# Kernel tuning notes

Hardware: AMD Instinct MI355X
Metric: run time of the kernel (lower is better)

Reference implementation:

```python
import jax, jax.numpy as jnp
import numpy as np

B, S, D = 1, 2048, 4096
N_Q, N_KV, HD = 32, 8, 128
N_REP = N_Q // N_KV
WINDOW = 1024
NEG = -1e9


def setup_inputs() -> dict:
    key = jax.random.key(0)
    ks = jax.random.split(key, 6)
    x = jax.random.normal(ks[0], (B, S, D), dtype=jnp.float32)
    # RoPE frequencies (Llama-style): theta = 10000^{-2i/HD}
    inv_freq = 1.0 / (10000.0 ** (np.arange(0, HD, 2, dtype=np.float32) / HD))
    t = np.arange(S, dtype=np.float32)
    ang = np.outer(t, inv_freq)  # [S, HD//2]
    freqs_cos = jnp.asarray(np.cos(ang), dtype=jnp.float32)
    freqs_sin = jnp.asarray(np.sin(ang), dtype=jnp.float32)
    # additive causal mask [S, S]: 0 on/below diag, -1e9 above
    mask = jnp.where(jnp.tril(jnp.ones((S, S), dtype=bool)), 0.0, NEG).astype(jnp.float32)
    scale = 0.02
    w_q = jax.random.normal(ks[1], (D, N_Q * HD), dtype=jnp.float32) * scale
    w_k = jax.random.normal(ks[2], (D, N_KV * HD), dtype=jnp.float32) * scale
    w_v = jax.random.normal(ks[3], (D, N_KV * HD), dtype=jnp.float32) * scale
    w_o = jax.random.normal(ks[4], (N_Q * HD, D), dtype=jnp.float32) * scale
    return {"x": x, "freqs_cos": freqs_cos, "freqs_sin": freqs_sin, "mask": mask,
            "w_q": w_q, "w_k": w_k, "w_v": w_v, "w_o": w_o}


def _rope(t, cos, sin):
    # t: [B, S, H, HD]; cos/sin: [S, HD//2] -> complex multiply on pairs
    tp = t.reshape(*t.shape[:-1], HD // 2, 2)
    e, o = tp[..., 0], tp[..., 1]
    c = cos[None, :, None, :]
    s = sin[None, :, None, :]
    re = e * c - o * s
    ro = e * s + o * c
    return jnp.stack([re, ro], axis=-1).reshape(t.shape)


def reference(x, freqs_cos, freqs_sin, mask, w_q, w_k, w_v, w_o):
    b, s, _ = x.shape
    xq = (x @ w_q).reshape(b, s, N_Q, HD)
    xk = (x @ w_k).reshape(b, s, N_KV, HD)
    xv = (x @ w_v).reshape(b, s, N_KV, HD)
    xq = _rope(xq, freqs_cos, freqs_sin)
    xk = _rope(xk, freqs_cos, freqs_sin)
    # GQA head repeat
    keys = jnp.repeat(xk, N_REP, axis=2)    # [b, s, N_Q, HD]
    values = jnp.repeat(xv, N_REP, axis=2)
    q = xq.transpose(0, 2, 1, 3)            # [b, h, s, hd]
    k = keys.transpose(0, 2, 1, 3)
    v = values.transpose(0, 2, 1, 3)
    scores = jnp.einsum('bhqd,bhkd->bhqk', q, k) / jnp.sqrt(jnp.float32(HD))
    scores = scores + mask[None, None, :, :]
    # sliding-window band: attend only to keys within WINDOW positions back
    idx = jnp.arange(s)
    diff = idx[:, None] - idx[None, :]
    sliding = (diff >= 0) & (diff < WINDOW)
    scores = jnp.where(sliding[None, None, :, :], scores, NEG)
    probs = jax.nn.softmax(scores, axis=-1).astype(q.dtype)
    out = jnp.einsum('bhqk,bhkd->bhqd', probs, v)
    out = out.transpose(0, 2, 1, 3).reshape(b, s, N_Q * HD)
    return out @ w_o
```

## Files before the change

### kernel.cpp

```cpp
#include <hip/hip_runtime.h>

typedef unsigned short u16;
typedef unsigned int u32;
typedef __bf16 bf16x8 __attribute__((ext_vector_type(8)));
typedef __bf16 bf16x4 __attribute__((ext_vector_type(4)));
typedef float f32x4 __attribute__((ext_vector_type(4)));

#define MFMA16(a, b, c) __builtin_amdgcn_mfma_f32_16x16x32_bf16(a, b, c, 0, 0, 0)

__device__ __forceinline__ u16 f2bf(float f) {
  u32 u = __float_as_uint(f);
  u += 0x7FFFu + ((u >> 16) & 1u);
  return (u16)(u >> 16);
}
__device__ __forceinline__ float bf2f(u16 h) {
  return __uint_as_float(((u32)h) << 16);
}

__device__ __forceinline__ void gload_lds16(const u16* g, u16* l) {
  __builtin_amdgcn_global_load_lds((__attribute__((address_space(1))) void*)g,
                                   (__attribute__((address_space(3))) void*)l,
                                   16, 0, 0);
}

__global__ __launch_bounds__(256) void cvt_x(const float* __restrict__ in,
                                             u16* __restrict__ out) {
  int i = (blockIdx.x * 256 + threadIdx.x) * 4;
  float4 v = *(const float4*)&in[i];
  ushort4 o;
  o.x = f2bf(v.x);
  o.y = f2bf(v.y);
  o.z = f2bf(v.z);
  o.w = f2bf(v.w);
  *(ushort4*)&out[i] = o;
}

__global__ __launch_bounds__(256) void tbf_f2b(const float* __restrict__ in,
                                               u16* __restrict__ out,
                                               int ldin, int ldout) {
  __shared__ float tile[64][65];
  const int t = threadIdx.x;
  const int c4 = t & 15;
  const int rb = t >> 4;
  const int r0 = blockIdx.y * 64;
  const int c0 = blockIdx.x * 64;
#pragma unroll
  for (int p = 0; p < 4; p++) {
    int r = p * 16 + rb;
    float4 v = *(const float4*)&in[(size_t)(r0 + r) * ldin + c0 + c4 * 4];
    tile[r][c4 * 4 + 0] = v.x;
    tile[r][c4 * 4 + 1] = v.y;
    tile[r][c4 * 4 + 2] = v.z;
    tile[r][c4 * 4 + 3] = v.w;
  }
  __syncthreads();
#pragma unroll
  for (int p = 0; p < 4; p++) {
    int oc = p * 16 + rb;
    ushort4 v;
    v.x = f2bf(tile[c4 * 4 + 0][oc]);
    v.y = f2bf(tile[c4 * 4 + 1][oc]);
    v.z = f2bf(tile[c4 * 4 + 2][oc]);
    v.w = f2bf(tile[c4 * 4 + 3][oc]);
    *(ushort4*)&out[(size_t)(c0 + oc) * ldout + r0 + c4 * 4] = v;
  }
}

__global__ __launch_bounds__(256) void tbf_b(const u16* __restrict__ in,
                                             u16* __restrict__ out,
                                             int ldin, int ldout) {
  __shared__ u16 tile[64][68];
  const int t = threadIdx.x;
  const int c4 = t & 15;
  const int rb = t >> 4;
  const int r0 = blockIdx.y * 64;
  const int c0 = blockIdx.x * 64;
#pragma unroll
  for (int p = 0; p < 4; p++) {
    int r = p * 16 + rb;
    ushort4 v = *(const ushort4*)&in[(size_t)(r0 + r) * ldin + c0 + c4 * 4];
    *(ushort4*)&tile[r][c4 * 4] = v;
  }
  __syncthreads();
#pragma unroll
  for (int p = 0; p < 4; p++) {
    int oc = p * 16 + rb;
    ushort4 v;
    v.x = tile[c4 * 4 + 0][oc];
    v.y = tile[c4 * 4 + 1][oc];
    v.z = tile[c4 * 4 + 2][oc];
    v.w = tile[c4 * 4 + 3][oc];
    *(ushort4*)&out[(size_t)(c0 + oc) * ldout + r0 + c4 * 4] = v;
  }
}

template <int BN, int F32OUT>
__global__ __launch_bounds__(512, 2) void gemmp(const u16* __restrict__ A,
                                                const u16* __restrict__ B,
                                                void* __restrict__ Cv,
                                                int K, int ldc) {
  constexpr int BM = 256;
  constexpr int R = 4;
  constexpr int C = BN / 32;
  constexpr int CH = C / 2;
  constexpr int LA = BM / 64;
  constexpr int LB = BN / 64;
  __shared__ __attribute__((aligned(16))) u16 As[2][BM * 64];
  __shared__ __attribute__((aligned(16))) u16 Bs[2][BN * 64];
  const int tid = threadIdx.x;
  const int wave = tid >> 6;
  const int lane = tid & 63;
  const int l16 = lane & 15;
  const int quad = lane >> 4;
  const int wm = wave >> 1;
  const int wn = wave & 1;
  const int id = blockIdx.x;
  const int bm = (id & 7) * BM;
  const int bn0 = (id >> 3) * BN;

  const u16* srcA[LA];
#pragma unroll
  for (int m = 0; m < LA; m++) {
    int c = m * 512 + tid;
    int r = c >> 3;
    int hl = (c & 7) ^ (r & 7);
    srcA[m] = A + (size_t)(bm + r) * K + hl * 8;
  }
  const u16* srcB[LB];
#pragma unroll
  for (int m = 0; m < LB; m++) {
    int c = m * 512 + tid;
    int r = c >> 3;
    int hl = (c & 7) ^ (r & 7);
    srcB[m] = B + (size_t)(bn0 + r) * K + hl * 8;
  }

  f32x4 acc[R][C];
#pragma unroll
  for (int i = 0; i < R; i++)
#pragma unroll
    for (int j = 0; j < C; j++) acc[i][j] = (f32x4){0.f, 0.f, 0.f, 0.f};

  auto stage = [&](int ko, int buf) {
#pragma unroll
    for (int m = 0; m < LA; m++)
      gload_lds16(srcA[m] + ko, &As[buf][(m * 512 + tid) * 8]);
#pragma unroll
    for (int m = 0; m < LB; m++)
      gload_lds16(srcB[m] + ko, &Bs[buf][(m * 512 + tid) * 8]);
  };

  const int NT = K >> 6;
  stage(0, 0);
  for (int t = 0; t < NT; ++t) {
    if (t + 1 < NT) {
      stage((t + 1) << 6, (t + 1) & 1);
      if constexpr (LA + LB == 7)
        asm volatile("s_waitcnt vmcnt(7)" ::: "memory");
      else
        asm volatile("s_waitcnt vmcnt(6)" ::: "memory");
    } else {
      asm volatile("s_waitcnt vmcnt(0)" ::: "memory");
    }
    __builtin_amdgcn_sched_barrier(0);
    __builtin_amdgcn_s_barrier();
    __builtin_amdgcn_sched_barrier(0);

    const u16* as = &As[t & 1][0];
    const u16* bs = &Bs[t & 1][0];
    bf16x8 afr[R];
#pragma unroll
    for (int ks = 0; ks < 2; ks++) {
#pragma unroll
      for (int ph = 0; ph < 2; ph++) {
        if (ph == 0) {
#pragma unroll
          for (int i = 0; i < R; i++) {
            int row = wm * 64 + i * 16 + l16;
            afr[i] = *(const bf16x8*)
                &as[row * 64 + (((ks * 4 + quad) ^ (row & 7)) << 3)];
          }
        }
        bf16x8 bfr[CH];
#pragma unroll
        for (int j = 0; j < CH; j++) {
          int row = wn * (C * 16) + (ph * CH + j) * 16 + l16;
          bfr[j] = *(const bf16x8*)
              &bs[row * 64 + (((ks * 4 + quad) ^ (row & 7)) << 3)];
        }
        __builtin_amdgcn_s_setprio(1);
#pragma unroll
        for (int i = 0; i < R; i++)
#pragma unroll
          for (int j = 0; j < CH; j++)
            acc[i][ph * CH + j] = MFMA16(afr[i], bfr[j], acc[i][ph * CH + j]);
        __builtin_amdgcn_s_setprio(0);
        __builtin_amdgcn_sched_barrier(0);
        __builtin_amdgcn_s_barrier();
        __builtin_amdgcn_sched_barrier(0);
      }
    }
  }

  const int crow0 = bm + wm * 64;
  const int ccol0 = bn0 + wn * (C * 16);
  if constexpr (F32OUT) {
    float* Cp = (float*)Cv;
#pragma unroll
    for (int i = 0; i < R; i++)
#pragma unroll
      for (int j = 0; j < C; j++)
#pragma unroll
        for (int rr = 0; rr < 4; rr++) {
          int row = crow0 + i * 16 + quad * 4 + rr;
          int col = ccol0 + j * 16 + l16;
          Cp[(size_t)row * ldc + col] = acc[i][j][rr];
        }
  } else {
    u16* Cp = (u16*)Cv;
#pragma unroll
    for (int i = 0; i < R; i++)
#pragma unroll
      for (int j = 0; j < C; j++)
#pragma unroll
        for (int rr = 0; rr < 4; rr++) {
          int row = crow0 + i * 16 + quad * 4 + rr;
          int col = ccol0 + j * 16 + l16;
          Cp[(size_t)row * ldc + col] = f2bf(acc[i][j][rr]);
        }
  }
}

__global__ __launch_bounds__(256) void rope_k(u16* __restrict__ qkv,
                                              const float* __restrict__ fc,
                                              const float* __restrict__ fs) {
  int idx = blockIdx.x * 256 + threadIdx.x;
  int j = idx & 63;
  int rem = idx >> 6;
  int head = rem % 40;
  int s = rem / 40;
  float c = fc[s * 64 + j];
  float sn = fs[s * 64 + j];
  int col = (head < 32) ? (head * 128 + 2 * j) : (4096 + (head - 32) * 128 + 2 * j);
  u32* p = (u32*)&qkv[(size_t)s * 6144 + col];
  u32 v = *p;
  float e = bf2f((u16)(v & 0xFFFFu));
  float o = bf2f((u16)(v >> 16));
  float re = e * c - o * sn;
  float ro = e * sn + o * c;
  *p = (u32)f2bf(re) | ((u32)f2bf(ro) << 16);
}

__global__ __launch_bounds__(256) void attn_k(const u16* __restrict__ qkv,
                                              const u16* __restrict__ vt,
                                              u16* __restrict__ outb) {
  __shared__ __attribute__((aligned(16))) u16 Kb[2][32 * 128];
  __shared__ __attribute__((aligned(16))) u16 Vb[2][128 * 32];
  __shared__ __attribute__((aligned(16))) u16 plds[4][32 * 36];
  const int h = blockIdx.x;
  const int q0 = blockIdx.y * 128;
  const int t = threadIdx.x;
  const int wave = t >> 6;
  const int lane = t & 63;
  const int l16 = lane & 15;
  const int quad = lane >> 4;
  const int hkv = h >> 2;
  const int qw = q0 + wave * 32;
  u16* myp = &plds[wave][0];

  bf16x8 qa[2][4];
#pragma unroll
  for (int i = 0; i < 2; i++)
#pragma unroll
    for (int kc = 0; kc < 4; kc++)
      qa[i][kc] = *(const bf16x8*)&qkv[(size_t)(qw + i * 16 + l16) * 6144 +
                                       h * 128 + kc * 32 + quad * 8];

  f32x4 o[2][8];
#pragma unroll
  for (int i = 0; i < 2; i++)
#pragma unroll
    for (int d = 0; d < 8; d++) o[i][d] = (f32x4){0.f, 0.f, 0.f, 0.f};
  float lloc[2][4] = {{0.f, 0.f, 0.f, 0.f}, {0.f, 0.f, 0.f, 0.f}};

  const int kb_start = (q0 - 1023 > 0 ? q0 - 1023 : 0) & ~31;
  const int kb_last = q0 + 96;
  const float sc = 0.08838834764831845f;

  const int kr0 = t >> 4, kc0s = t & 15;
  const int kr1 = (256 + t) >> 4, kc1s = t & 15;
  const int vr0 = t >> 2, vc0s = t & 3;
  const int vr1 = (256 + t) >> 2, vc1s = t & 3;
  const u16* kg = qkv + 4096 + hkv * 128;
  const u16* vg = vt + (size_t)hkv * 128 * 2048;

#define STAGE(kb_, nb_)                                                        \
  do {                                                                         \
    int kb__ = (kb_);                                                          \
    gload_lds16(&kg[(size_t)(kb__ + kr0) * 6144 + (kc0s ^ (kr0 & 15)) * 8],    \
                &Kb[nb_][t * 8]);                                              \
    gload_lds16(&kg[(size_t)(kb__ + kr1) * 6144 + (kc1s ^ (kr1 & 15)) * 8],    \
                &Kb[nb_][2048 + t * 8]);                                       \
    gload_lds16(&vg[(size_t)vr0 * 2048 + kb__ + (vc0s ^ (vr0 & 3)) * 8],       \
                &Vb[nb_][t * 8]);                                              \
    gload_lds16(&vg[(size_t)vr1 * 2048 + kb__ + (vc1s ^ (vr1 & 3)) * 8],       \
                &Vb[nb_][2048 + t * 8]);                                       \
  } while (0)

  STAGE(kb_start, 0);
  int cur = 0;

  for (int kb = kb_start; kb <= kb_last; kb += 32) {
    __syncthreads();
    if (kb + 32 <= kb_last) STAGE(kb + 32, cur ^ 1);
    const u16* kcur = &Kb[cur][0];
    const u16* vcur = &Vb[cur][0];

    f32x4 s0[2] = {(f32x4){0.f, 0.f, 0.f, 0.f}, (f32x4){0.f, 0.f, 0.f, 0.f}};
    f32x4 s1[2] = {(f32x4){0.f, 0.f, 0.f, 0.f}, (f32x4){0.f, 0.f, 0.f, 0.f}};
#pragma unroll
    for (int kc = 0; kc < 4; kc++) {
      int ch = ((kc * 4 + quad) ^ l16) * 8;
      bf16x8 b0 = *(const bf16x8*)&kcur[l16 * 128 + ch];
      bf16x8 b1 = *(const bf16x8*)&kcur[(l16 + 16) * 128 + ch];
      s0[0] = MFMA16(qa[0][kc], b0, s0[0]);
      s1[0] = MFMA16(qa[0][kc], b1, s1[0]);
      s0[1] = MFMA16(qa[1][kc], b0, s0[1]);
      s1[1] = MFMA16(qa[1][kc], b1, s1[1]);
    }

    float p0[2][4], p1[2][4];
    bool fast = (kb + 31 <= qw) && (qw + 31 - kb <= 1023);
    if (fast) {
#pragma unroll
      for (int i = 0; i < 2; i++)
#pragma unroll
        for (int r = 0; r < 4; r++) {
          p0[i][r] = __expf(s0[i][r] * sc);
          p1[i][r] = __expf(s1[i][r] * sc);
        }
    } else {
#pragma unroll
      for (int i = 0; i < 2; i++)
#pragma unroll
        for (int r = 0; r < 4; r++) {
          int row = qw + i * 16 + quad * 4 + r;
          int col0 = kb + l16;
          int col1 = col0 + 16;
          bool v0 = (col0 <= row) && (row - col0 < 1024);
          bool v1 = (col1 <= row) && (row - col1 < 1024);
          p0[i][r] = v0 ? __expf(s0[i][r] * sc) : 0.f;
          p1[i][r] = v1 ? __expf(s1[i][r] * sc) : 0.f;
        }
    }
#pragma unroll
    for (int i = 0; i < 2; i++)
#pragma unroll
      for (int r = 0; r < 4; r++) {
        lloc[i][r] += p0[i][r] + p1[i][r];
        myp[(i * 16 + quad * 4 + r) * 36 + l16] = f2bf(p0[i][r]);
        myp[(i * 16 + quad * 4 + r) * 36 + l16 + 16] = f2bf(p1[i][r]);
      }
    asm volatile("s_waitcnt lgkmcnt(0)" ::: "memory");
    bf16x8 pa[2];
#pragma unroll
    for (int i = 0; i < 2; i++) {
      bf16x4 lo = *(const bf16x4*)&myp[(i * 16 + l16) * 36 + quad * 8];
      bf16x4 hi = *(const bf16x4*)&myp[(i * 16 + l16) * 36 + quad * 8 + 4];
#pragma unroll
      for (int j = 0; j < 4; j++) {
        pa[i][j] = lo[j];
        pa[i][j + 4] = hi[j];
      }
    }
#pragma unroll
    for (int d = 0; d < 8; d++) {
      int rv = l16 + 16 * d;
      bf16x8 vb = *(const bf16x8*)&vcur[rv * 32 + ((quad ^ (l16 & 3)) * 8)];
      o[0][d] = MFMA16(pa[0], vb, o[0][d]);
      o[1][d] = MFMA16(pa[1], vb, o[1][d]);
    }
    cur ^= 1;
  }

#pragma unroll
  for (int i = 0; i < 2; i++) {
    float inv[4];
#pragma unroll
    for (int r = 0; r < 4; r++) {
      float l = lloc[i][r];
#pragma unroll
      for (int m = 8; m >= 1; m >>= 1) l += __shfl_xor(l, m, 64);
      inv[r] = 1.0f / l;
    }
#pragma unroll
    for (int d = 0; d < 8; d++)
#pragma unroll
      for (int r = 0; r < 4; r++) {
        int row = qw + i * 16 + quad * 4 + r;
        outb[(size_t)row * 4096 + h * 128 + d * 16 + l16] =
            f2bf(o[i][d][r] * inv[r]);
      }
  }
#undef STAGE
}

extern "C" void kernel_launch(void* const* d_in, const int* in_sizes, int n_in,
                              void* d_out, int out_size, void* d_ws, size_t ws_size,
                              hipStream_t stream) {
  const float* x = (const float*)d_in[0];
  const float* fc = (const float*)d_in[1];
  const float* fs = (const float*)d_in[2];
  const float* wq = (const float*)d_in[4];
  const float* wk = (const float*)d_in[5];
  const float* wv = (const float*)d_in[6];
  const float* wo = (const float*)d_in[7];
  float* outp = (float*)d_out;
  char* ws = (char*)d_ws;
  u16* xb = (u16*)(ws);
  u16* wqkvT = (u16*)(ws + 16777216);
  u16* qkvb = (u16*)(ws + 67108864);
  u16* vtb = (u16*)(ws + 92274688);
  u16* aout = (u16*)(ws + 96468992);

  cvt_x<<<8192, 256, 0, stream>>>(x, xb);
  tbf_f2b<<<dim3(64, 64), 256, 0, stream>>>(wq, wqkvT, 4096, 4096);
  tbf_f2b<<<dim3(16, 64), 256, 0, stream>>>(wk, wqkvT + (size_t)4096 * 4096,
                                            1024, 4096);
  tbf_f2b<<<dim3(16, 64), 256, 0, stream>>>(wv, wqkvT + (size_t)5120 * 4096,
                                            1024, 4096);
  gemmp<192, 0><<<256, 512, 0, stream>>>(xb, wqkvT, qkvb, 4096, 6144);
  rope_k<<<20480, 256, 0, stream>>>(qkvb, fc, fs);
  tbf_b<<<dim3(16, 32), 256, 0, stream>>>(qkvb + 5120, vtb, 6144, 2048);
  tbf_f2b<<<dim3(64, 64), 256, 0, stream>>>(wo, wqkvT, 4096, 4096);
  attn_k<<<dim3(32, 16), 256, 0, stream>>>(qkvb, vtb, aout);
  gemmp<128, 1><<<256, 512, 0, stream>>>(aout, wqkvT, outp, 4096, 4096);
}
```

Measured before the change: 526.7 us.

## Restructure GEMM into 8-phase interleaved load/MFMA schedule with 2x4 wave layout

Replaces the double-buffered GEMM main loop with a hand-scheduled eight-phase ping-pong. Each phase issues a fraction of the next tile's global-to-LDS loads between register fragment reads and an MFMA cluster, with explicit barriers and vmcnt waits. Waves are regrouped as 2x4, so each wave computes 128 rows by NC*16 columns, which changes fragment reuse. The aim is to hide global load latency and LDS reads behind MFMA work. In exchange, the per-wave accumulator count grows and the wait counts are fragile and must match the issued loads exactly.

New measurement: 481.0 us. 1.1x faster.

```diff
diff --git a/kernel.cpp b/kernel.cpp
--- a/kernel.cpp
+++ b/kernel.cpp
@@ -95,140 +95,229 @@
 }
 
 template <int BN, int F32OUT>
-__global__ __launch_bounds__(512, 2) void gemmp(const u16* __restrict__ A,
+__global__ __launch_bounds__(512, 2) void gemm8(const u16* __restrict__ A,
                                                 const u16* __restrict__ B,
                                                 void* __restrict__ Cv,
                                                 int K, int ldc) {
-  constexpr int BM = 256;
-  constexpr int R = 4;
-  constexpr int C = BN / 32;
-  constexpr int CH = C / 2;
-  constexpr int LA = BM / 64;
-  constexpr int LB = BN / 64;
-  __shared__ __attribute__((aligned(16))) u16 As[2][BM * 64];
+  constexpr int NC = BN / 64;
+  __shared__ __attribute__((aligned(16))) u16 As[2][256 * 64];
   __shared__ __attribute__((aligned(16))) u16 Bs[2][BN * 64];
   const int tid = threadIdx.x;
   const int wave = tid >> 6;
   const int lane = tid & 63;
   const int l16 = lane & 15;
   const int quad = lane >> 4;
-  const int wm = wave >> 1;
-  const int wn = wave & 1;
+  const int wm = wave >> 2;
+  const int wc = wave & 3;
   const int id = blockIdx.x;
-  const int bm = (id & 7) * BM;
+  const int bm = (id & 7) * 256;
   const int bn0 = (id >> 3) * BN;
 
-  const u16* srcA[LA];
-#pragma unroll
-  for (int m = 0; m < LA; m++) {
+  const u16* srcA[4];
+#pragma unroll
+  for (int m = 0; m < 4; m++) {
     int c = m * 512 + tid;
     int r = c >> 3;
     int hl = (c & 7) ^ (r & 7);
     srcA[m] = A + (size_t)(bm + r) * K + hl * 8;
   }
-  const u16* srcB[LB];
-#pragma unroll
-  for (int m = 0; m < LB; m++) {
+  const u16* srcB[NC];
+#pragma unroll
+  for (int m = 0; m < NC; m++) {
     int c = m * 512 + tid;
     int r = c >> 3;
     int hl = (c & 7) ^ (r & 7);
     srcB[m] = B + (size_t)(bn0 + r) * K + hl * 8;
   }
 
-  f32x4 acc[R][C];
-#pragma unroll
-  for (int i = 0; i < R; i++)
-#pragma unroll
-    for (int j = 0; j < C; j++) acc[i][j] = (f32x4){0.f, 0.f, 0.f, 0.f};
-
-  auto stage = [&](int ko, int buf) {
-#pragma unroll
-    for (int m = 0; m < LA; m++)
-      gload_lds16(srcA[m] + ko, &As[buf][(m * 512 + tid) * 8]);
-#pragma unroll
-    for (int m = 0; m < LB; m++)
-      gload_lds16(srcB[m] + ko, &Bs[buf][(m * 512 + tid) * 8]);
+  f32x4 acc[8][NC];
+#pragma unroll
+  for (int i = 0; i < 8; i++)
+#pragma unroll
+    for (int j = 0; j < NC; j++) acc[i][j] = (f32x4){0.f, 0.f, 0.f, 0.f};
+
+#define STA(u, koff, buf) \
+  gload_lds16(srcA[u] + (koff), &As[buf][((u) * 512 + tid) * 8])
+#define STB(u, koff, buf) \
+  gload_lds16(srcB[u] + (koff), &Bs[buf][((u) * 512 + tid) * 8])
+#define SB __builtin_amdgcn_sched_barrier(0)
+#define MID                                          \
+  SB;                                                \
+  __builtin_amdgcn_s_barrier();                      \
+  asm volatile("s_waitcnt lgkmcnt(0)" ::: "memory"); \
+  SB
+#define END                     \
+  SB;                           \
+  __builtin_amdgcn_s_barrier(); \
+  SB
+
+  bf16x8 aR[2][4], bR0[NC], bR1[NC];
+  auto rdA = [&](const u16* s, int mh) {
+#pragma unroll
+    for (int ks = 0; ks < 2; ks++)
+#pragma unroll
+      for (int ii = 0; ii < 4; ii++) {
+        int row = wm * 128 + mh * 64 + ii * 16 + l16;
+        aR[ks][ii] = *(const bf16x8*)
+            &s[row * 64 + (((ks * 4 + quad) ^ (row & 7)) << 3)];
+      }
   };
-
-  const int NT = K >> 6;
-  stage(0, 0);
-  for (int t = 0; t < NT; ++t) {
-    if (t + 1 < NT) {
-      stage((t + 1) << 6, (t + 1) & 1);
-      if constexpr (LA + LB == 7)
-        asm volatile("s_waitcnt vmcnt(7)" ::: "memory");
+  auto rdB = [&](const u16* s, int ks, bf16x8(&bR)[NC]) {
+#pragma unroll
+    for (int j = 0; j < NC; j++) {
+      int row = wc * (NC * 16) + j * 16 + l16;
+      bR[j] = *(const bf16x8*)
+          &s[row * 64 + (((ks * 4 + quad) ^ (row & 7)) << 3)];
+    }
+  };
+  auto cl = [&](bf16x8(&a4)[4], bf16x8(&bR)[NC], int mh) {
+    __builtin_amdgcn_s_setprio(1);
+#pragma unroll
+    for (int ii = 0; ii < 4; ii++)
+#pragma unroll
+      for (int j = 0; j < NC; j++)
+        acc[mh * 4 + ii][j] = MFMA16(a4[ii], bR[j], acc[mh * 4 + ii][j]);
+    __builtin_amdgcn_s_setprio(0);
+  };
+
+#pragma unroll
+  for (int u = 0; u < 4; u++) STA(u, 0, 0);
+#pragma unroll
+  for (int u = 0; u < NC; u++) STB(u, 0, 0);
+#pragma unroll
+  for (int u = 0; u < NC; u++) STB(u, 64, 1);
+  if constexpr (NC == 3)
+    asm volatile("s_waitcnt vmcnt(3)" ::: "memory");
+  else
+    asm volatile("s_waitcnt vmcnt(2)" ::: "memory");
+  END;
+
+  const int NP = K >> 7;
+  for (int p = 0; p < NP; ++p) {
+    const int kT1 = p * 128 + 64;
+    const int kT2 = p * 128 + 128;
+    const int kT3 = p * 128 + 192;
+    const bool more = (p + 1 < NP);
+    const u16* as0 = &As[0][0];
+    const u16* bs0 = &Bs[0][0];
+    const u16* as1 = &As[1][0];
+    const u16* bs1 = &Bs[1][0];
+
+    rdA(as0, 0);
+    rdB(bs0, 0, bR0);
+    STA(0, kT1, 1);
+    STA(1, kT1, 1);
+    MID;
+    cl(aR[0], bR0, 0);
+    END;
+    rdB(bs0, 1, bR1);
+    STA(2, kT1, 1);
+    STA(3, kT1, 1);
+    MID;
+    cl(aR[1], bR1, 0);
+    END;
+    rdA(as0, 1);
+    if (more) {
+      STB(0, kT2, 0);
+      STB(1, kT2, 0);
+    }
+    MID;
+    cl(aR[1], bR1, 1);
+    END;
+    if (more) {
+      if constexpr (NC == 3) {
+        STB(2, kT2, 0);
+        STA(0, kT2, 0);
+      } else {
+        STA(0, kT2, 0);
+        STA(1, kT2, 0);
+      }
+    }
+    MID;
+    cl(aR[0], bR0, 1);
+    SB;
+    if (more)
+      asm volatile("s_waitcnt vmcnt(4)" ::: "memory");
+    else
+      asm volatile("s_waitcnt vmcnt(0)" ::: "memory");
+    END;
+
+    rdA(as1, 0);
+    rdB(bs1, 0, bR0);
+    if (more) {
+      if constexpr (NC == 3) {
+        STA(1, kT2, 0);
+        STA(2, kT2, 0);
+      } else {
+        STA(2, kT2, 0);
+        STA(3, kT2, 0);
+      }
+    }
+    MID;
+    cl(aR[0], bR0, 0);
+    END;
+    rdB(bs1, 1, bR1);
+    if (more) {
+      if constexpr (NC == 3) STA(3, kT2, 0);
+    }
+    MID;
+    cl(aR[1], bR1, 0);
+    END;
+    rdA(as1, 1);
+    if (more) {
+      STB(0, kT3, 1);
+      STB(1, kT3, 1);
+    }
+    MID;
+    cl(aR[1], bR1, 1);
+    END;
+    if (more) {
+      if constexpr (NC == 3) STB(2, kT3, 1);
+    }
+    MID;
+    cl(aR[0], bR0, 1);
+    SB;
+    if (more) {
+      if constexpr (NC == 3)
+        asm volatile("s_waitcnt vmcnt(3)" ::: "memory");
       else
-        asm volatile("s_waitcnt vmcnt(6)" ::: "memory");
-    } else {
-      asm volatile("s_waitcnt vmcnt(0)" ::: "memory");
-    }
-    __builtin_amdgcn_sched_barrier(0);
-    __builtin_amdgcn_s_barrier();
-    __builtin_amdgcn_sched_barrier(0);
-
-    const u16* as = &As[t & 1][0];
-    const u16* bs = &Bs[t & 1][0];
-    bf16x8 afr[R];
-#pragma unroll
-    for (int ks = 0; ks < 2; ks++) {
-#pragma unroll
-      for (int ph = 0; ph < 2; ph++) {
-        if (ph == 0) {
-#pragma unroll
-          for (int i = 0; i < R; i++) {
-            int row = wm * 64 + i * 16 + l16;
-            afr[i] = *(const bf16x8*)
-                &as[row * 64 + (((ks * 4 + quad) ^ (row & 7)) << 3)];
-          }
-        }
-        bf16x8 bfr[CH];
-#pragma unroll
-        for (int j = 0; j < CH; j++) {
-          int row = wn * (C * 16) + (ph * CH + j) * 16 + l16;
-          bfr[j] = *(const bf16x8*)
-              &bs[row * 64 + (((ks * 4 + quad) ^ (row & 7)) << 3)];
-        }
-        __builtin_amdgcn_s_setprio(1);
-#pragma unroll
-        for (int i = 0; i < R; i++)
-#pragma unroll
-          for (int j = 0; j < CH; j++)
-            acc[i][ph * CH + j] = MFMA16(afr[i], bfr[j], acc[i][ph * CH + j]);
-        __builtin_amdgcn_s_setprio(0);
-        __builtin_amdgcn_sched_barrier(0);
-        __builtin_amdgcn_s_barrier();
-        __builtin_amdgcn_sched_barrier(0);
-      }
-    }
-  }
-
-  const int crow0 = bm + wm * 64;
-  const int ccol0 = bn0 + wn * (C * 16);
+        asm volatile("s_waitcnt vmcnt(2)" ::: "memory");
+    }
+    END;
+  }
+
+  const int crow0 = bm + wm * 128;
+  const int ccol0 = bn0 + wc * (NC * 16);
   if constexpr (F32OUT) {
     float* Cp = (float*)Cv;
 #pragma unroll
-    for (int i = 0; i < R; i++)
-#pragma unroll
-      for (int j = 0; j < C; j++)
+    for (int r8 = 0; r8 < 8; r8++)
+#pragma unroll
+      for (int j = 0; j < NC; j++)
 #pragma unroll
         for (int rr = 0; rr < 4; rr++) {
-          int row = crow0 + i * 16 + quad * 4 + rr;
+          int row = crow0 + (r8 >> 2) * 64 + (r8 & 3) * 16 + quad * 4 + rr;
           int col = ccol0 + j * 16 + l16;
-          Cp[(size_t)row * ldc + col] = acc[i][j][rr];
+          Cp[(size_t)row * ldc + col] = acc[r8][j][rr];
         }
   } else {
     u16* Cp = (u16*)Cv;
 #pragma unroll
-    for (int i = 0; i < R; i++)
-#pragma unroll
-      for (int j = 0; j < C; j++)
+    for (int r8 = 0; r8 < 8; r8++)
+#pragma unroll
+      for (int j = 0; j < NC; j++)
 #pragma unroll
         for (int rr = 0; rr < 4; rr++) {
-          int row = crow0 + i * 16 + quad * 4 + rr;
+          int row = crow0 + (r8 >> 2) * 64 + (r8 & 3) * 16 + quad * 4 + rr;
           int col = ccol0 + j * 16 + l16;
-          Cp[(size_t)row * ldc + col] = f2bf(acc[i][j][rr]);
+          Cp[(size_t)row * ldc + col] = f2bf(acc[r8][j][rr]);
         }
   }
+#undef STA
+#undef STB
+#undef SB
+#undef MID
+#undef END
 }
 
 __global__ __launch_bounds__(256) void rope_k(u16* __restrict__ qkv,
@@ -429,10 +518,10 @@
                                             1024, 4096);
   tbf_f2b<<<dim3(16, 64), 256, 0, stream>>>(wv, wqkvT + (size_t)5120 * 4096,
                                             1024, 4096);
-  gemmp<192, 0><<<256, 512, 0, stream>>>(xb, wqkvT, qkvb, 4096, 6144);
+  gemm8<192, 0><<<256, 512, 0, stream>>>(xb, wqkvT, qkvb, 4096, 6144);
   rope_k<<<20480, 256, 0, stream>>>(qkvb, fc, fs);
   tbf_b<<<dim3(16, 32), 256, 0, stream>>>(qkvb + 5120, vtb, 6144, 2048);
   tbf_f2b<<<dim3(64, 64), 256, 0, stream>>>(wo, wqkvT, 4096, 4096);
   attn_k<<<dim3(32, 16), 256, 0, stream>>>(qkvb, vtb, aout);
-  gemmp<128, 1><<<256, 512, 0, stream>>>(aout, wqkvT, outp, 4096, 4096);
-}
+  gemm8<128, 1><<<256, 512, 0, stream>>>(aout, wqkvT, outp, 4096, 4096);
+}
```

## Rewrite projection GEMMs to use 32x32 MFMA with 4-wave blocks

Applied to the files above, without the earlier changes.

Replaces the 8-wave 16x16x32 MFMA GEMM with a 4-wave kernel that gives each wave a 128xBN/2 tile computed with 32x32x16 bf16 MFMA. It also changes the LDS swizzle to include a second XOR term and drops the intra-tile barriers, keeping one barrier per K step. The goal is fewer LDS fragment reads per FLOP and higher MFMA throughput. The cost is larger accumulator register pressure, lower wave count per CU, and less latency hiding with launch bounds of 256 threads and 1 block.

Result: no change. 536.4 us (+1.9%).

```diff
diff --git a/kernel.cpp b/kernel.cpp
--- a/kernel.cpp
+++ b/kernel.cpp
@@ -5,8 +5,10 @@
 typedef __bf16 bf16x8 __attribute__((ext_vector_type(8)));
 typedef __bf16 bf16x4 __attribute__((ext_vector_type(4)));
 typedef float f32x4 __attribute__((ext_vector_type(4)));
+typedef float f32x16 __attribute__((ext_vector_type(16)));
 
 #define MFMA16(a, b, c) __builtin_amdgcn_mfma_f32_16x16x32_bf16(a, b, c, 0, 0, 0)
+#define MFMA32(a, b, c) __builtin_amdgcn_mfma_f32_32x32x16_bf16(a, b, c, 0, 0, 0)
 
 __device__ __forceinline__ u16 f2bf(float f) {
   u32 u = __float_as_uint(f);
@@ -95,59 +97,59 @@
 }
 
 template <int BN, int F32OUT>
-__global__ __launch_bounds__(512, 2) void gemmp(const u16* __restrict__ A,
-                                                const u16* __restrict__ B,
-                                                void* __restrict__ Cv,
-                                                int K, int ldc) {
-  constexpr int BM = 256;
-  constexpr int R = 4;
-  constexpr int C = BN / 32;
-  constexpr int CH = C / 2;
-  constexpr int LA = BM / 64;
-  constexpr int LB = BN / 64;
-  __shared__ __attribute__((aligned(16))) u16 As[2][BM * 64];
+__global__ __launch_bounds__(256, 1) void gemw(const u16* __restrict__ A,
+                                               const u16* __restrict__ B,
+                                               void* __restrict__ Cv,
+                                               int K, int ldc) {
+  constexpr int NC = BN / 64;
+  constexpr int UA = 8;
+  constexpr int UB = BN / 32;
+  constexpr int LL = UA + UB;
+  __shared__ __attribute__((aligned(16))) u16 As[2][256 * 64];
   __shared__ __attribute__((aligned(16))) u16 Bs[2][BN * 64];
   const int tid = threadIdx.x;
   const int wave = tid >> 6;
   const int lane = tid & 63;
-  const int l16 = lane & 15;
-  const int quad = lane >> 4;
+  const int l32 = lane & 31;
+  const int hk = lane >> 5;
   const int wm = wave >> 1;
-  const int wn = wave & 1;
+  const int wc = wave & 1;
   const int id = blockIdx.x;
-  const int bm = (id & 7) * BM;
+  const int bm = (id & 7) * 256;
   const int bn0 = (id >> 3) * BN;
 
-  const u16* srcA[LA];
-#pragma unroll
-  for (int m = 0; m < LA; m++) {
-    int c = m * 512 + tid;
+  const u16* srcA[UA];
+#pragma unroll
+  for (int m = 0; m < UA; m++) {
+    int c = m * 256 + tid;
     int r = c >> 3;
-    int hl = (c & 7) ^ (r & 7);
+    int hl = (c & 7) ^ (r & 7) ^ ((r >> 3) & 3);
     srcA[m] = A + (size_t)(bm + r) * K + hl * 8;
   }
-  const u16* srcB[LB];
-#pragma unroll
-  for (int m = 0; m < LB; m++) {
-    int c = m * 512 + tid;
+  const u16* srcB[UB];
+#pragma unroll
+  for (int m = 0; m < UB; m++) {
+    int c = m * 256 + tid;
     int r = c >> 3;
-    int hl = (c & 7) ^ (r & 7);
+    int hl = (c & 7) ^ (r & 7) ^ ((r >> 3) & 3);
     srcB[m] = B + (size_t)(bn0 + r) * K + hl * 8;
   }
 
-  f32x4 acc[R][C];
-#pragma unroll
-  for (int i = 0; i < R; i++)
-#pragma unroll
-    for (int j = 0; j < C; j++) acc[i][j] = (f32x4){0.f, 0.f, 0.f, 0.f};
+  f32x16 acc[4][NC];
+#pragma unroll
+  for (int i = 0; i < 4; i++)
+#pragma unroll
+    for (int j = 0; j < NC; j++)
+#pragma unroll
+      for (int e = 0; e < 16; e++) acc[i][j][e] = 0.f;
 
   auto stage = [&](int ko, int buf) {
 #pragma unroll
-    for (int m = 0; m < LA; m++)
-      gload_lds16(srcA[m] + ko, &As[buf][(m * 512 + tid) * 8]);
-#pragma unroll
-    for (int m = 0; m < LB; m++)
-      gload_lds16(srcB[m] + ko, &Bs[buf][(m * 512 + tid) * 8]);
+    for (int m = 0; m < UA; m++)
+      gload_lds16(srcA[m] + ko, &As[buf][(m * 256 + tid) * 8]);
+#pragma unroll
+    for (int m = 0; m < UB; m++)
+      gload_lds16(srcB[m] + ko, &Bs[buf][(m * 256 + tid) * 8]);
   };
 
   const int NT = K >> 6;
@@ -155,10 +157,10 @@
   for (int t = 0; t < NT; ++t) {
     if (t + 1 < NT) {
       stage((t + 1) << 6, (t + 1) & 1);
-      if constexpr (LA + LB == 7)
-        asm volatile("s_waitcnt vmcnt(7)" ::: "memory");
+      if constexpr (LL == 14)
+        asm volatile("s_waitcnt vmcnt(14)" ::: "memory");
       else
-        asm volatile("s_waitcnt vmcnt(6)" ::: "memory");
+        asm volatile("s_waitcnt vmcnt(12)" ::: "memory");
     } else {
       asm volatile("s_waitcnt vmcnt(0)" ::: "memory");
     }
@@ -168,65 +170,59 @@
 
     const u16* as = &As[t & 1][0];
     const u16* bs = &Bs[t & 1][0];
-    bf16x8 afr[R];
-#pragma unroll
-    for (int ks = 0; ks < 2; ks++) {
-#pragma unroll
-      for (int ph = 0; ph < 2; ph++) {
-        if (ph == 0) {
-#pragma unroll
-          for (int i = 0; i < R; i++) {
-            int row = wm * 64 + i * 16 + l16;
-            afr[i] = *(const bf16x8*)
-                &as[row * 64 + (((ks * 4 + quad) ^ (row & 7)) << 3)];
-          }
-        }
-        bf16x8 bfr[CH];
-#pragma unroll
-        for (int j = 0; j < CH; j++) {
-          int row = wn * (C * 16) + (ph * CH + j) * 16 + l16;
-          bfr[j] = *(const bf16x8*)
-              &bs[row * 64 + (((ks * 4 + quad) ^ (row & 7)) << 3)];
-        }
-        __builtin_amdgcn_s_setprio(1);
-#pragma unroll
-        for (int i = 0; i < R; i++)
-#pragma unroll
-          for (int j = 0; j < CH; j++)
-            acc[i][ph * CH + j] = MFMA16(afr[i], bfr[j], acc[i][ph * CH + j]);
-        __builtin_amdgcn_s_setprio(0);
-        __builtin_amdgcn_sched_barrier(0);
-        __builtin_amdgcn_s_barrier();
-        __builtin_amdgcn_sched_barrier(0);
+#pragma unroll
+    for (int ks = 0; ks < 4; ks++) {
+      bf16x8 aF[4], bF[NC];
+#pragma unroll
+      for (int i = 0; i < 4; i++) {
+        int r = wm * 128 + i * 32 + l32;
+        int pc = (ks * 2 + hk) ^ (r & 7) ^ ((r >> 3) & 3);
+        aF[i] = *(const bf16x8*)&as[r * 64 + pc * 8];
       }
-    }
-  }
-
-  const int crow0 = bm + wm * 64;
-  const int ccol0 = bn0 + wn * (C * 16);
+#pragma unroll
+      for (int j = 0; j < NC; j++) {
+        int r = wc * (NC * 32) + j * 32 + l32;
+        int pc = (ks * 2 + hk) ^ (r & 7) ^ ((r >> 3) & 3);
+        bF[j] = *(const bf16x8*)&bs[r * 64 + pc * 8];
+      }
+      __builtin_amdgcn_s_setprio(1);
+#pragma unroll
+      for (int i = 0; i < 4; i++)
+#pragma unroll
+        for (int j = 0; j < NC; j++)
+          acc[i][j] = MFMA32(aF[i], bF[j], acc[i][j]);
+      __builtin_amdgcn_s_setprio(0);
+    }
+    __builtin_amdgcn_sched_barrier(0);
+    __builtin_amdgcn_s_barrier();
+    __builtin_amdgcn_sched_barrier(0);
+  }
+
+  const int crow0 = bm + wm * 128;
+  const int ccol0 = bn0 + wc * (NC * 32);
   if constexpr (F32OUT) {
     float* Cp = (float*)Cv;
 #pragma unroll
-    for (int i = 0; i < R; i++)
-#pragma unroll
-      for (int j = 0; j < C; j++)
-#pragma unroll
-        for (int rr = 0; rr < 4; rr++) {
-          int row = crow0 + i * 16 + quad * 4 + rr;
-          int col = ccol0 + j * 16 + l16;
-          Cp[(size_t)row * ldc + col] = acc[i][j][rr];
+    for (int i = 0; i < 4; i++)
+#pragma unroll
+      for (int j = 0; j < NC; j++)
+#pragma unroll
+        for (int reg = 0; reg < 16; reg++) {
+          int row = crow0 + i * 32 + (reg & 3) + 8 * (reg >> 2) + 4 * hk;
+          int col = ccol0 + j * 32 + l32;
+          Cp[(size_t)row * ldc + col] = acc[i][j][reg];
         }
   } else {
     u16* Cp = (u16*)Cv;
 #pragma unroll
-    for (int i = 0; i < R; i++)
-#pragma unroll
-      for (int j = 0; j < C; j++)
-#pragma unroll
-        for (int rr = 0; rr < 4; rr++) {
-          int row = crow0 + i * 16 + quad * 4 + rr;
-          int col = ccol0 + j * 16 + l16;
-          Cp[(size_t)row * ldc + col] = f2bf(acc[i][j][rr]);
+    for (int i = 0; i < 4; i++)
+#pragma unroll
+      for (int j = 0; j < NC; j++)
+#pragma unroll
+        for (int reg = 0; reg < 16; reg++) {
+          int row = crow0 + i * 32 + (reg & 3) + 8 * (reg >> 2) + 4 * hk;
+          int col = ccol0 + j * 32 + l32;
+          Cp[(size_t)row * ldc + col] = f2bf(acc[i][j][reg]);
         }
   }
 }
@@ -429,10 +425,10 @@
                                             1024, 4096);
   tbf_f2b<<<dim3(16, 64), 256, 0, stream>>>(wv, wqkvT + (size_t)5120 * 4096,
                                             1024, 4096);
-  gemmp<192, 0><<<256, 512, 0, stream>>>(xb, wqkvT, qkvb, 4096, 6144);
+  gemw<192, 0><<<256, 256, 0, stream>>>(xb, wqkvT, qkvb, 4096, 6144);
   rope_k<<<20480, 256, 0, stream>>>(qkvb, fc, fs);
   tbf_b<<<dim3(16, 32), 256, 0, stream>>>(qkvb + 5120, vtb, 6144, 2048);
   tbf_f2b<<<dim3(64, 64), 256, 0, stream>>>(wo, wqkvT, 4096, 4096);
   attn_k<<<dim3(32, 16), 256, 0, stream>>>(qkvb, vtb, aout);
-  gemmp<128, 1><<<256, 512, 0, stream>>>(aout, wqkvT, outp, 4096, 4096);
-}
+  gemw<128, 1><<<256, 256, 0, stream>>>(aout, wqkvT, outp, 4096, 4096);
+}
```
